# Performance work log

Hardware: AMD Instinct MI355X
Metric: run time of the kernel (lower is better)

## Reference

```python
import jax, jax.numpy as jnp
import numpy as np

D_MODEL = 2048
N_HEADS = 16
D_HEAD = D_MODEL // N_HEADS
B, S = 4, 2048


def setup_inputs() -> dict:
    key = jax.random.key(0)
    ks = jax.random.split(key, 5)
    scale = 1.0 / np.sqrt(D_MODEL)
    return {
        "x": jax.random.normal(ks[0], (B, S, D_MODEL), dtype=jnp.float32),
        "w_qkv": jax.random.normal(ks[1], (D_MODEL, 3 * D_MODEL), dtype=jnp.float32) * scale,
        "b_qkv": jax.random.normal(ks[2], (3 * D_MODEL,), dtype=jnp.float32) * 0.01,
        "w_out": jax.random.normal(ks[3], (D_MODEL, D_MODEL), dtype=jnp.float32) * scale,
        "b_out": jax.random.normal(ks[4], (D_MODEL,), dtype=jnp.float32) * 0.01,
    }


def reference(x, w_qkv, b_qkv, w_out, b_out):
    b, s, d = x.shape
    qkv = x @ w_qkv + b_qkv                      # [b, s, 3d]
    q, k, v = jnp.split(qkv, 3, axis=-1)
    # [b, h, s, dh]
    q = q.reshape(b, s, N_HEADS, D_HEAD).transpose(0, 2, 1, 3)
    k = k.reshape(b, s, N_HEADS, D_HEAD).transpose(0, 2, 1, 3)
    v = v.reshape(b, s, N_HEADS, D_HEAD).transpose(0, 2, 1, 3)
    # past_kv is None -> s_past == s
    scale = 1.0 / np.sqrt(D_HEAD).astype(np.float32)
    scores = jnp.einsum("bhqd,bhkd->bhqk", q, k) * scale  # [b, h, s, s]
    # causal mask: disallow j > i (diagonal = 1 + s_past - s = 1)
    causal = jnp.tril(jnp.ones((s, s), dtype=bool))
    scores = jnp.where(causal, scores, jnp.float32(-jnp.inf))
    attn = jax.nn.softmax(scores, axis=-1)
    out = jnp.einsum("bhqk,bhkd->bhqd", attn, v)          # [b, h, s, dh]
    out = out.transpose(0, 2, 1, 3).reshape(b, s, d)
    out = out @ w_out + b_out
    return out, k, v
```

## Files before the change

### kernel.cpp

```cpp
#include <hip/hip_runtime.h>
#include <hip/hip_bf16.h>
#include <cstdint>

typedef unsigned short u16;
typedef unsigned int u32;
typedef __attribute__((ext_vector_type(4))) float f32x4;
typedef __attribute__((ext_vector_type(8))) __bf16 bf16x8;

#define DEVFN static __device__ __forceinline__

constexpr int Bb = 4, S = 2048, Dm = 2048, H = 16, DH = 128;
constexpr int M  = Bb * S;
constexpr int N3 = 3 * Dm;
constexpr int KK = 2048;
constexpr float ATTN_SCALE = 0.088388347648318447f;
constexpr float LOG2E = 1.4426950408889634f;

DEVFN u16 f2bf(float f) {
  union { float f; u32 u; } v; v.f = f;
  u32 u = v.u;
  return (u16)((u + 0x7fffu + ((u >> 16) & 1u)) >> 16);
}

DEVFN void async16(const void* g, void* l) {
  __builtin_amdgcn_global_load_lds(
      (__attribute__((address_space(1))) unsigned int*)(g),
      (__attribute__((address_space(3))) unsigned int*)(l), 16, 0, 0);
}


DEVFN void transpose_tile(const float* __restrict__ in, u16* __restrict__ out,
                          int R, int C, int bx, int by, int tid) {
  __shared__ float tile[32][33];
  int c0 = bx * 32, r0 = by * 32;
  int tx = tid & 31, ty = tid >> 5;
#pragma unroll
  for (int i = 0; i < 4; i++)
    tile[ty + 8 * i][tx] = in[(size_t)(r0 + ty + 8 * i) * C + c0 + tx];
  __syncthreads();
  int tx2 = (tid & 7) * 4, ty2 = tid >> 3;
  ushort4 o;
  o.x = f2bf(tile[tx2 + 0][ty2]);
  o.y = f2bf(tile[tx2 + 1][ty2]);
  o.z = f2bf(tile[tx2 + 2][ty2]);
  o.w = f2bf(tile[tx2 + 3][ty2]);
  *(ushort4*)(&out[(size_t)(c0 + ty2) * R + r0 + tx2]) = o;
}

__global__ __launch_bounds__(256) void k_prep(
    const float* __restrict__ x, const float* __restrict__ w_qkv,
    const float* __restrict__ w_out, u16* __restrict__ x_bf,
    u16* __restrict__ wqkvT, u16* __restrict__ woutT) {
  const int bid = blockIdx.x, tid = threadIdx.x;
  constexpr int NB_CVT = (M * Dm) / 1024;
  constexpr int NB_T1 = (N3 / 32) * (Dm / 32);
  if (bid < NB_CVT) {
    int i = (bid * 256 + tid) * 4;
    float4 f = *(const float4*)(x + i);
    ushort4 o;
    o.x = f2bf(f.x); o.y = f2bf(f.y); o.z = f2bf(f.z); o.w = f2bf(f.w);
    *(ushort4*)(x_bf + i) = o;
  } else if (bid < NB_CVT + NB_T1) {
    int b2 = bid - NB_CVT;
    transpose_tile(w_qkv, wqkvT, Dm, N3, b2 % (N3 / 32), b2 / (N3 / 32), tid);
  } else {
    int b3 = bid - NB_CVT - NB_T1;
    transpose_tile(w_out, woutT, Dm, Dm, b3 % (Dm / 32), b3 / (Dm / 32), tid);
  }
}


#define RA(buf, half) ((buf) * 65536 + (half) * 16384)
#define RB(buf, half) ((buf) * 65536 + 32768 + (half) * 16384)

#define BARRIER() __builtin_amdgcn_s_barrier()
#define SCHEDB() __builtin_amdgcn_sched_barrier(0)
#define LGK0() { asm volatile("s_waitcnt lgkmcnt(0)" ::: "memory"); __builtin_amdgcn_sched_barrier(0); }
#define VMC0() { asm volatile("s_waitcnt vmcnt(0)" ::: "memory"); __builtin_amdgcn_sched_barrier(0); }

template <int BUF, int QUAD>
DEVFN void ldAq(const char* lds, int wm, int lrow, int lkg, bf16x8 af[4][2]) {
  const char* base = lds + RA(BUF, 0) + wm * 16384;
  const int sw = (lrow & 7) << 4;
#pragma unroll
  for (int mi = 0; mi < 4; mi++) {
    int row = QUAD * 64 + mi * 16 + lrow;
#pragma unroll
    for (int kk = 0; kk < 2; kk++)
      af[mi][kk] = *(const bf16x8*)(base + row * 128 + ((kk * 64 + lkg * 16) ^ sw));
  }
}

template <int BUF, int NS>
DEVFN void ldB(const char* lds, int wn, int lrow, int lkg, bf16x8 b[2][2]) {
  const char* base = lds + RB(BUF, 0) + (wn >> 1) * 16384;
  const int sw = (lrow & 7) << 4;
#pragma unroll
  for (int ni = 0; ni < 2; ni++) {
    int row = (wn & 1) * 64 + NS * 32 + ni * 16 + lrow;
#pragma unroll
    for (int kk = 0; kk < 2; kk++)
      b[ni][kk] = *(const bf16x8*)(base + row * 128 + ((kk * 64 + lkg * 16) ^ sw));
  }
}

template <int MS, int NS>
DEVFN void mmq(f32x4 acc[8][4], bf16x8 af[4][2], bf16x8 b[2][2]) {
  __builtin_amdgcn_s_setprio(1);
#pragma unroll
  for (int kk = 0; kk < 2; kk++)
#pragma unroll
    for (int mi = 0; mi < 4; mi++)
#pragma unroll
      for (int ni = 0; ni < 2; ni++)
        acc[MS * 4 + mi][NS * 2 + ni] = __builtin_amdgcn_mfma_f32_16x16x32_bf16(
            af[mi][kk], b[ni][kk], acc[MS * 4 + mi][NS * 2 + ni], 0, 0, 0);
  __builtin_amdgcn_s_setprio(0);
}

template <int MODE>
__global__ __launch_bounds__(512, 2) void k_gemm(
    const u16* __restrict__ A, const u16* __restrict__ BT,
    const float* __restrict__ bias, float* __restrict__ Cf,
    u16* __restrict__ q_bf, u16* __restrict__ k_bf, u16* __restrict__ v_bfT,
    int N) {
  __shared__ __align__(16) char lds[131072];
  char* ldsc = lds;
  const int tid = threadIdx.x;
  const int wid = tid >> 6, lane = tid & 63;
  const int wm = wid >> 2, wn = wid & 3;
  const int lrow = lane & 15, lkg = lane >> 4;

  const int bid = blockIdx.x;
  const int xcd = bid & 7;
  const int i = bid >> 3;
  const int r = i & 15;
  const int j = i >> 4;
  const int tm0 = (xcd * 4 + (r >> 2)) << 8;
  const int tn0 = (j * 4 + (r & 3)) << 8;

  const int NT = KK >> 6;

  const int srow = tid >> 3;
  const int scol = (((tid & 7) * 16) ^ ((srow & 7) << 4)) >> 1;
  const int dstoff = (tid & ~63) * 16;
  const u16* bA0 = A + (size_t)(tm0 + srow) * KK + scol;
  const u16* bA1 = A + (size_t)(tm0 + 128 + srow) * KK + scol;
  const u16* bB0 = BT + (size_t)(tn0 + srow) * KK + scol;
  const u16* bB1 = BT + (size_t)(tn0 + 128 + srow) * KK + scol;

  auto stage2 = [&](const u16* src, int region) {
    async16(src, ldsc + region + dstoff);
    async16(src + (size_t)64 * KK, ldsc + region + 8192 + dstoff);
  };

  f32x4 acc[8][4] = {};
  bf16x8 afA[4][2], afB[4][2], b0[2][2], b1[2][2];

  stage2(bA0, RA(0, 0));
  stage2(bA1, RA(0, 1));
  stage2(bB0, RB(0, 0));
  stage2(bB1, RB(0, 1));
  VMC0();
  BARRIER();

  for (int it = 0; it < NT / 2; it++) {
    const int t = 2 * it;
    const int t1 = (t + 1) * 64;
    const int t2 = (t + 2 < NT) ? (t + 2) * 64 : 0;

    ldAq<0, 0>(ldsc, wm, lrow, lkg, afA);
    ldB<0, 0>(ldsc, wn, lrow, lkg, b0);
    stage2(bA0 + t1, RA(1, 0));
    stage2(bB0 + t1, RB(1, 0));
    SCHEDB();
    BARRIER(); LGK0();
    mmq<0, 0>(acc, afA, b0);

    ldB<0, 1>(ldsc, wn, lrow, lkg, b1);
    stage2(bA1 + t1, RA(1, 1));
    stage2(bB1 + t1, RB(1, 1));
    SCHEDB();
    BARRIER(); LGK0();
    mmq<0, 1>(acc, afA, b1);

    ldAq<0, 1>(ldsc, wm, lrow, lkg, afB);
    SCHEDB();
    BARRIER(); LGK0();
    mmq<1, 1>(acc, afB, b1);

    VMC0();
    BARRIER();
    mmq<1, 0>(acc, afB, b0);

    ldAq<1, 0>(ldsc, wm, lrow, lkg, afA);
    ldB<1, 0>(ldsc, wn, lrow, lkg, b0);
    stage2(bA0 + t2, RA(0, 0));
    stage2(bB0 + t2, RB(0, 0));
    SCHEDB();
    BARRIER(); LGK0();
    mmq<0, 0>(acc, afA, b0);

    ldB<1, 1>(ldsc, wn, lrow, lkg, b1);
    stage2(bA1 + t2, RA(0, 1));
    stage2(bB1 + t2, RB(0, 1));
    SCHEDB();
    BARRIER(); LGK0();
    mmq<0, 1>(acc, afA, b1);

    ldAq<1, 1>(ldsc, wm, lrow, lkg, afB);
    SCHEDB();
    BARRIER(); LGK0();
    mmq<1, 1>(acc, afB, b1);

    VMC0();
    BARRIER();
    mmq<1, 0>(acc, afB, b0);
  }

  if (MODE == 0) {
#pragma unroll
    for (int mig = 0; mig < 8; mig++) {
      int row = tm0 + wm * 128 + (mig >> 2) * 64 + (mig & 3) * 16 + lkg * 4;
#pragma unroll
      for (int nig = 0; nig < 4; nig++) {
        int col = tn0 + wn * 64 + (nig >> 1) * 32 + (nig & 1) * 16 + lrow;
        float bv = bias[col];
#pragma unroll
        for (int r2 = 0; r2 < 4; r2++)
          Cf[(size_t)(row + r2) * N + col] = acc[mig][nig][r2] + bv;
      }
    }
  } else {
#pragma unroll
    for (int mig = 0; mig < 8; mig++) {
      int row = tm0 + wm * 128 + (mig >> 2) * 64 + (mig & 3) * 16 + lkg * 4;
#pragma unroll
      for (int nig = 0; nig < 4; nig++) {
        int n = tn0 + wn * 64 + (nig >> 1) * 32 + (nig & 1) * 16 + lrow;
        float bv = bias[n];
        int type = n >> 11;
        int d = n & 2047;
        int h = d >> 7, dh = d & 127;
#pragma unroll
        for (int r2 = 0; r2 < 4; r2++) {
          int rr = row + r2;
          int b = rr >> 11, s = rr & 2047;
          float val = acc[mig][nig][r2] + bv;
          size_t idx = ((size_t)(b * H + h) * S + s) * DH + dh;
          if (type == 0) {
            q_bf[idx] = f2bf(val * ATTN_SCALE);
          } else if (type == 1) {
            Cf[(size_t)M * Dm + idx] = val;
            k_bf[idx] = f2bf(val);
          } else {
            Cf[(size_t)2 * M * Dm + idx] = val;
            v_bfT[((size_t)(b * H + h) * DH + dh) * S + s] = f2bf(val);
          }
        }
      }
    }
  }
}

__global__ __launch_bounds__(256, 2) void k_attn(const u16* __restrict__ q_bf,
                                                 const u16* __restrict__ k_bf,
                                                 const u16* __restrict__ v_bfT,
                                                 u16* __restrict__ attn_bf) {
  __shared__ u16 ldsK[2][64 * 128];
  __shared__ u16 ldsV[2][128 * 64];
  __shared__ u16 ldsP[4][32 * 64];

  const int tid = threadIdx.x;
  const int wid = tid >> 6, lane = tid & 63;
  const int lrow = lane & 15, lkg = lane >> 4;

  const int bid = blockIdx.x;
  const int xcd = bid & 7;
  const int ii = bid >> 3;
  const int bh = xcd * 8 + (ii >> 4);
  const int qi = 15 - (ii & 15);
  const int b = bh >> 4, h = bh & 15;
  const int wq0 = qi * 128 + wid * 32;
  const int swz = (lrow & 7) << 4;

  const u16* qp = q_bf + (size_t)bh * S * DH;
  const u16* kp = k_bf + (size_t)bh * S * DH;
  const u16* vp = v_bfT + (size_t)bh * DH * S;

  bf16x8 qf[2][4];
#pragma unroll
  for (int qt = 0; qt < 2; qt++)
#pragma unroll
    for (int kk = 0; kk < 4; kk++)
      qf[qt][kk] = *(const bf16x8*)(qp + (size_t)(wq0 + qt * 16 + lrow) * DH +
                                    kk * 32 + lkg * 8);

  float mr[2][4], lr[2][4];
#pragma unroll
  for (int qt = 0; qt < 2; qt++)
#pragma unroll
    for (int r = 0; r < 4; r++) { mr[qt][r] = -1e30f; lr[qt][r] = 0.f; }
  f32x4 oacc[2][8] = {};

  const int nkb = qi * 2 + 2;

  auto stage = [&](int kb, int buf) {
#pragma unroll
    for (int i = 0; i < 4; i++) {
      int L = i * 4096 + wid * 1024 + lane * 16;
      int krow = L >> 8, kch = (L >> 4) & 15;
      async16(kp + (size_t)(kb * 64 + krow) * DH + ((kch ^ (krow & 7)) * 8),
              (char*)ldsK[buf] + L);
      int vd = L >> 7, vch = (L >> 4) & 7;
      async16(vp + (size_t)vd * S + kb * 64 + ((vch ^ (vd & 7)) * 8),
              (char*)ldsV[buf] + L);
    }
  };

  stage(0, 0);
  asm volatile("s_waitcnt vmcnt(0)" ::: "memory");
  __builtin_amdgcn_s_barrier();

  int cur = 0;
  for (int kb = 0; kb < nkb; kb++) {
    if (kb + 1 < nkb) stage(kb + 1, cur ^ 1);

    if (kb * 64 <= wq0 + 31) {
      const u16* Kc = ldsK[cur];
      const u16* Vc = ldsV[cur];
      f32x4 sacc[2][4] = {};
      __builtin_amdgcn_s_setprio(1);
#pragma unroll
      for (int kt = 0; kt < 4; kt++)
#pragma unroll
        for (int kk = 0; kk < 4; kk++) {
          bf16x8 kf = *(const bf16x8*)((const char*)Kc +
                        (kt * 16 + lrow) * 256 + ((kk * 64 + lkg * 16) ^ swz));
          sacc[0][kt] = __builtin_amdgcn_mfma_f32_16x16x32_bf16(qf[0][kk], kf,
                                                                sacc[0][kt], 0, 0, 0);
          sacc[1][kt] = __builtin_amdgcn_mfma_f32_16x16x32_bf16(qf[1][kk], kf,
                                                                sacc[1][kt], 0, 0, 0);
        }
      __builtin_amdgcn_s_setprio(0);

      if (kb * 64 + 63 > wq0) {
#pragma unroll
        for (int qt = 0; qt < 2; qt++)
#pragma unroll
          for (int kt = 0; kt < 4; kt++) {
            int k = kb * 64 + kt * 16 + lrow;
#pragma unroll
            for (int r = 0; r < 4; r++)
              if (k > wq0 + qt * 16 + lkg * 4 + r) sacc[qt][kt][r] = -1e30f;
          }
      }

      float pm[2][4];
#pragma unroll
      for (int qt = 0; qt < 2; qt++)
#pragma unroll
        for (int r = 0; r < 4; r++)
          pm[qt][r] = fmaxf(fmaxf(sacc[qt][0][r], sacc[qt][1][r]),
                            fmaxf(sacc[qt][2][r], sacc[qt][3][r]));
#pragma unroll
      for (int off = 1; off < 16; off <<= 1)
#pragma unroll
        for (int qt = 0; qt < 2; qt++)
#pragma unroll
          for (int r = 0; r < 4; r++)
            pm[qt][r] = fmaxf(pm[qt][r], __shfl_xor(pm[qt][r], off, 64));

      float dmax = pm[0][0] - mr[0][0];
#pragma unroll
      for (int qt = 0; qt < 2; qt++)
#pragma unroll
        for (int r = 0; r < 4; r++)
          dmax = fmaxf(dmax, pm[qt][r] - mr[qt][r]);
      if (!__all(dmax <= 8.0f)) {
        float sc[2][4];
#pragma unroll
        for (int qt = 0; qt < 2; qt++)
#pragma unroll
          for (int r = 0; r < 4; r++) {
            float mn = fmaxf(mr[qt][r], pm[qt][r]);
            sc[qt][r] = exp2f((mr[qt][r] - mn) * LOG2E);
            mr[qt][r] = mn;
            lr[qt][r] *= sc[qt][r];
          }
#pragma unroll
        for (int qt = 0; qt < 2; qt++)
#pragma unroll
          for (int nd = 0; nd < 8; nd++)
#pragma unroll
            for (int r = 0; r < 4; r++) oacc[qt][nd][r] *= sc[qt][r];
      }

      float rs[2][4] = {};
#pragma unroll
      for (int qt = 0; qt < 2; qt++)
#pragma unroll
        for (int kt = 0; kt < 4; kt++)
#pragma unroll
          for (int r = 0; r < 4; r++) {
            float p = exp2f((sacc[qt][kt][r] - mr[qt][r]) * LOG2E);
            rs[qt][r] += p;
            int prow = qt * 16 + lkg * 4 + r;
            *(u16*)((char*)ldsP[wid] + prow * 128 +
                    (((kt * 16 + lrow) * 2) ^ ((prow & 7) << 4))) = f2bf(p);
          }
#pragma unroll
      for (int off = 1; off < 16; off <<= 1)
#pragma unroll
        for (int qt = 0; qt < 2; qt++)
#pragma unroll
          for (int r = 0; r < 4; r++)
            rs[qt][r] += __shfl_xor(rs[qt][r], off, 64);
#pragma unroll
      for (int qt = 0; qt < 2; qt++)
#pragma unroll
        for (int r = 0; r < 4; r++)
          lr[qt][r] += rs[qt][r];

      asm volatile("s_waitcnt lgkmcnt(0)" ::: "memory");
      bf16x8 pf[2][2];
#pragma unroll
      for (int qt = 0; qt < 2; qt++)
#pragma unroll
        for (int kk = 0; kk < 2; kk++)
          pf[qt][kk] = *(const bf16x8*)((const char*)ldsP[wid] +
                         (qt * 16 + lrow) * 128 + ((kk * 64 + lkg * 16) ^ swz));
      __builtin_amdgcn_s_setprio(1);
#pragma unroll
      for (int nd = 0; nd < 8; nd++) {
        bf16x8 vf0 = *(const bf16x8*)((const char*)Vc +
                       (nd * 16 + lrow) * 128 + ((lkg * 16) ^ swz));
        bf16x8 vf1 = *(const bf16x8*)((const char*)Vc +
                       (nd * 16 + lrow) * 128 + ((64 + lkg * 16) ^ swz));
#pragma unroll
        for (int qt = 0; qt < 2; qt++) {
          oacc[qt][nd] = __builtin_amdgcn_mfma_f32_16x16x32_bf16(pf[qt][0], vf0,
                                                                 oacc[qt][nd], 0, 0, 0);
          oacc[qt][nd] = __builtin_amdgcn_mfma_f32_16x16x32_bf16(pf[qt][1], vf1,
                                                                 oacc[qt][nd], 0, 0, 0);
        }
      }
      __builtin_amdgcn_s_setprio(0);
    }

    asm volatile("s_waitcnt vmcnt(0)" ::: "memory");
    __builtin_amdgcn_s_barrier();
    cur ^= 1;
  }

#pragma unroll
  for (int qt = 0; qt < 2; qt++) {
    float inv[4];
#pragma unroll
    for (int r = 0; r < 4; r++) inv[r] = 1.0f / lr[qt][r];
#pragma unroll
    for (int nd = 0; nd < 8; nd++)
#pragma unroll
      for (int r = 0; r < 4; r++) {
        int q = wq0 + qt * 16 + lkg * 4 + r;
        size_t idx = ((size_t)(b * S + q) * H + h) * DH + nd * 16 + lrow;
        attn_bf[idx] = f2bf(oacc[qt][nd][r] * inv[r]);
      }
  }
}


extern "C" void kernel_launch(void* const* d_in, const int* in_sizes, int n_in,
                              void* d_out, int out_size, void* d_ws, size_t ws_size,
                              hipStream_t stream) {
  const float* x     = (const float*)d_in[0];
  const float* w_qkv = (const float*)d_in[1];
  const float* b_qkv = (const float*)d_in[2];
  const float* w_out = (const float*)d_in[3];
  const float* b_out = (const float*)d_in[4];
  float* out = (float*)d_out;

  char* ws = (char*)d_ws;
  u16* x_bf    = (u16*)ws; ws += (size_t)M * Dm * 2;
  u16* wqkvT   = (u16*)ws; ws += (size_t)N3 * Dm * 2;
  u16* woutT   = (u16*)ws; ws += (size_t)Dm * Dm * 2;
  u16* q_bf    = (u16*)ws; ws += (size_t)M * Dm * 2;
  u16* k_bf    = (u16*)ws; ws += (size_t)M * Dm * 2;
  u16* v_bfT   = (u16*)ws; ws += (size_t)M * Dm * 2;
  u16* attn_bf = (u16*)ws; ws += (size_t)M * Dm * 2;

  constexpr int NB_PREP = (M * Dm) / 1024 + (N3 / 32) * (Dm / 32) +
                          (Dm / 32) * (Dm / 32);
  k_prep<<<NB_PREP, 256, 0, stream>>>(x, w_qkv, w_out, x_bf, wqkvT, woutT);

  k_gemm<1><<<(N3 / 256) * (M / 256), 512, 0, stream>>>(
      x_bf, wqkvT, b_qkv, out, q_bf, k_bf, v_bfT, N3);

  k_attn<<<S / 128 * Bb * H, 256, 0, stream>>>(q_bf, k_bf, v_bfT, attn_bf);

  k_gemm<0><<<(Dm / 256) * (M / 256), 512, 0, stream>>>(
      attn_bf, woutT, b_out, out, nullptr, nullptr, nullptr, Dm);
}
```

Baseline: 545.7 us.

## Split GEMM blocks into sixteen waves with 64x64 per-wave tiles

Both GEMM kernels now launch 1024 threads per block instead of 512. Each of the 16 waves computes a 64x64 output sub-tile instead of 128x64, and each thread stages one 16-byte chunk per LDS region instead of two. LDS fragment loaders and the epilogue indexing are rewritten for the new wave-to-tile mapping. The aim is to lower per-wave register pressure and spread the global-to-LDS copies over more threads, at the cost of more LDS reads per MFMA, less register reuse, and barriers across more waves with only one block per CU.

```diff
diff --git a/kernel.cpp b/kernel.cpp
--- a/kernel.cpp
+++ b/kernel.cpp
@@ -78,48 +78,46 @@
 #define LGK0() { asm volatile("s_waitcnt lgkmcnt(0)" ::: "memory"); __builtin_amdgcn_sched_barrier(0); }
 #define VMC0() { asm volatile("s_waitcnt vmcnt(0)" ::: "memory"); __builtin_amdgcn_sched_barrier(0); }
 
-template <int BUF, int QUAD>
-DEVFN void ldAq(const char* lds, int wm, int lrow, int lkg, bf16x8 af[4][2]) {
-  const char* base = lds + RA(BUF, 0) + wm * 16384;
-  const int sw = (lrow & 7) << 4;
-#pragma unroll
-  for (int mi = 0; mi < 4; mi++) {
-    int row = QUAD * 64 + mi * 16 + lrow;
+template <int BUF, int MH>
+DEVFN void ldAh(const char* lds, int wm, int lrow, int lkg, bf16x8 af[2][2]) {
+  const char* base = lds + RA(BUF, 0);
+#pragma unroll
+  for (int mi = 0; mi < 2; mi++) {
+    int row = wm * 64 + MH * 32 + mi * 16 + lrow;
 #pragma unroll
     for (int kk = 0; kk < 2; kk++)
-      af[mi][kk] = *(const bf16x8*)(base + row * 128 + ((kk * 64 + lkg * 16) ^ sw));
-  }
-}
-
-template <int BUF, int NS>
-DEVFN void ldB(const char* lds, int wn, int lrow, int lkg, bf16x8 b[2][2]) {
-  const char* base = lds + RB(BUF, 0) + (wn >> 1) * 16384;
-  const int sw = (lrow & 7) << 4;
+      af[mi][kk] = *(const bf16x8*)(base + row * 128 + ((kk * 64 + lkg * 16) ^ ((row & 7) << 4)));
+  }
+}
+
+template <int BUF, int NH>
+DEVFN void ldBh(const char* lds, int wn, int lrow, int lkg, bf16x8 b[2][2]) {
+  const char* base = lds + RB(BUF, 0);
 #pragma unroll
   for (int ni = 0; ni < 2; ni++) {
-    int row = (wn & 1) * 64 + NS * 32 + ni * 16 + lrow;
+    int row = wn * 64 + NH * 32 + ni * 16 + lrow;
 #pragma unroll
     for (int kk = 0; kk < 2; kk++)
-      b[ni][kk] = *(const bf16x8*)(base + row * 128 + ((kk * 64 + lkg * 16) ^ sw));
-  }
-}
-
-template <int MS, int NS>
-DEVFN void mmq(f32x4 acc[8][4], bf16x8 af[4][2], bf16x8 b[2][2]) {
+      b[ni][kk] = *(const bf16x8*)(base + row * 128 + ((kk * 64 + lkg * 16) ^ ((row & 7) << 4)));
+  }
+}
+
+template <int MH, int NH>
+DEVFN void mmq(f32x4 acc[4][4], bf16x8 af[2][2], bf16x8 b[2][2]) {
   __builtin_amdgcn_s_setprio(1);
 #pragma unroll
   for (int kk = 0; kk < 2; kk++)
 #pragma unroll
-    for (int mi = 0; mi < 4; mi++)
+    for (int mi = 0; mi < 2; mi++)
 #pragma unroll
       for (int ni = 0; ni < 2; ni++)
-        acc[MS * 4 + mi][NS * 2 + ni] = __builtin_amdgcn_mfma_f32_16x16x32_bf16(
-            af[mi][kk], b[ni][kk], acc[MS * 4 + mi][NS * 2 + ni], 0, 0, 0);
+        acc[MH * 2 + mi][NH * 2 + ni] = __builtin_amdgcn_mfma_f32_16x16x32_bf16(
+            af[mi][kk], b[ni][kk], acc[MH * 2 + mi][NH * 2 + ni], 0, 0, 0);
   __builtin_amdgcn_s_setprio(0);
 }
 
 template <int MODE>
-__global__ __launch_bounds__(512, 2) void k_gemm(
+__global__ __launch_bounds__(1024) void k_gemm(
     const u16* __restrict__ A, const u16* __restrict__ BT,
     const float* __restrict__ bias, float* __restrict__ Cf,
     u16* __restrict__ q_bf, u16* __restrict__ k_bf, u16* __restrict__ v_bfT,
@@ -142,49 +140,47 @@
   const int NT = KK >> 6;
 
   const int srow = tid >> 3;
-  const int scol = (((tid & 7) * 16) ^ ((srow & 7) << 4)) >> 1;
+  const int scol = (((tid & 7) ^ ((tid >> 3) & 7)) << 3);
   const int dstoff = (tid & ~63) * 16;
   const u16* bA0 = A + (size_t)(tm0 + srow) * KK + scol;
   const u16* bA1 = A + (size_t)(tm0 + 128 + srow) * KK + scol;
   const u16* bB0 = BT + (size_t)(tn0 + srow) * KK + scol;
   const u16* bB1 = BT + (size_t)(tn0 + 128 + srow) * KK + scol;
 
-  auto stage2 = [&](const u16* src, int region) {
+  auto stage1 = [&](const u16* src, int region) {
     async16(src, ldsc + region + dstoff);
-    async16(src + (size_t)64 * KK, ldsc + region + 8192 + dstoff);
   };
 
-  f32x4 acc[8][4] = {};
-  bf16x8 afA[4][2], afB[4][2], b0[2][2], b1[2][2];
-
-  stage2(bA0, RA(0, 0));
-  stage2(bA1, RA(0, 1));
-  stage2(bB0, RB(0, 0));
-  stage2(bB1, RB(0, 1));
+  f32x4 acc[4][4] = {};
+  bf16x8 afA[2][2], afB[2][2], b0[2][2], b1[2][2];
+
+  stage1(bA0, RA(0, 0));
+  stage1(bA1, RA(0, 1));
+  stage1(bB0, RB(0, 0));
+  stage1(bB1, RB(0, 1));
   VMC0();
   BARRIER();
 
   for (int it = 0; it < NT / 2; it++) {
-    const int t = 2 * it;
-    const int t1 = (t + 1) * 64;
-    const int t2 = (t + 2 < NT) ? (t + 2) * 64 : 0;
-
-    ldAq<0, 0>(ldsc, wm, lrow, lkg, afA);
-    ldB<0, 0>(ldsc, wn, lrow, lkg, b0);
-    stage2(bA0 + t1, RA(1, 0));
-    stage2(bB0 + t1, RB(1, 0));
+    const int t1 = (2 * it + 1) * 64;
+    const int t2 = (2 * it + 2 < NT) ? (2 * it + 2) * 64 : 0;
+
+    ldAh<0, 0>(ldsc, wm, lrow, lkg, afA);
+    ldBh<0, 0>(ldsc, wn, lrow, lkg, b0);
+    stage1(bA0 + t1, RA(1, 0));
+    stage1(bB0 + t1, RB(1, 0));
     SCHEDB();
     BARRIER(); LGK0();
     mmq<0, 0>(acc, afA, b0);
 
-    ldB<0, 1>(ldsc, wn, lrow, lkg, b1);
-    stage2(bA1 + t1, RA(1, 1));
-    stage2(bB1 + t1, RB(1, 1));
+    ldBh<0, 1>(ldsc, wn, lrow, lkg, b1);
+    stage1(bA1 + t1, RA(1, 1));
+    stage1(bB1 + t1, RB(1, 1));
     SCHEDB();
     BARRIER(); LGK0();
     mmq<0, 1>(acc, afA, b1);
 
-    ldAq<0, 1>(ldsc, wm, lrow, lkg, afB);
+    ldAh<0, 1>(ldsc, wm, lrow, lkg, afB);
     SCHEDB();
     BARRIER(); LGK0();
     mmq<1, 1>(acc, afB, b1);
@@ -193,22 +189,22 @@
     BARRIER();
     mmq<1, 0>(acc, afB, b0);
 
-    ldAq<1, 0>(ldsc, wm, lrow, lkg, afA);
-    ldB<1, 0>(ldsc, wn, lrow, lkg, b0);
-    stage2(bA0 + t2, RA(0, 0));
-    stage2(bB0 + t2, RB(0, 0));
+    ldAh<1, 0>(ldsc, wm, lrow, lkg, afA);
+    ldBh<1, 0>(ldsc, wn, lrow, lkg, b0);
+    stage1(bA0 + t2, RA(0, 0));
+    stage1(bB0 + t2, RB(0, 0));
     SCHEDB();
     BARRIER(); LGK0();
     mmq<0, 0>(acc, afA, b0);
 
-    ldB<1, 1>(ldsc, wn, lrow, lkg, b1);
-    stage2(bA1 + t2, RA(0, 1));
-    stage2(bB1 + t2, RB(0, 1));
+    ldBh<1, 1>(ldsc, wn, lrow, lkg, b1);
+    stage1(bA1 + t2, RA(0, 1));
+    stage1(bB1 + t2, RB(0, 1));
     SCHEDB();
     BARRIER(); LGK0();
     mmq<0, 1>(acc, afA, b1);
 
-    ldAq<1, 1>(ldsc, wm, lrow, lkg, afB);
+    ldAh<1, 1>(ldsc, wm, lrow, lkg, afB);
     SCHEDB();
     BARRIER(); LGK0();
     mmq<1, 1>(acc, afB, b1);
@@ -220,24 +216,24 @@
 
   if (MODE == 0) {
 #pragma unroll
-    for (int mig = 0; mig < 8; mig++) {
-      int row = tm0 + wm * 128 + (mig >> 2) * 64 + (mig & 3) * 16 + lkg * 4;
-#pragma unroll
-      for (int nig = 0; nig < 4; nig++) {
-        int col = tn0 + wn * 64 + (nig >> 1) * 32 + (nig & 1) * 16 + lrow;
+    for (int mi = 0; mi < 4; mi++) {
+      int row = tm0 + wm * 64 + mi * 16 + lkg * 4;
+#pragma unroll
+      for (int ni = 0; ni < 4; ni++) {
+        int col = tn0 + wn * 64 + ni * 16 + lrow;
         float bv = bias[col];
 #pragma unroll
         for (int r2 = 0; r2 < 4; r2++)
-          Cf[(size_t)(row + r2) * N + col] = acc[mig][nig][r2] + bv;
+          Cf[(size_t)(row + r2) * N + col] = acc[mi][ni][r2] + bv;
       }
     }
   } else {
 #pragma unroll
-    for (int mig = 0; mig < 8; mig++) {
-      int row = tm0 + wm * 128 + (mig >> 2) * 64 + (mig & 3) * 16 + lkg * 4;
-#pragma unroll
-      for (int nig = 0; nig < 4; nig++) {
-        int n = tn0 + wn * 64 + (nig >> 1) * 32 + (nig & 1) * 16 + lrow;
+    for (int mi = 0; mi < 4; mi++) {
+      int row = tm0 + wm * 64 + mi * 16 + lkg * 4;
+#pragma unroll
+      for (int ni = 0; ni < 4; ni++) {
+        int n = tn0 + wn * 64 + ni * 16 + lrow;
         float bv = bias[n];
         int type = n >> 11;
         int d = n & 2047;
@@ -246,7 +242,7 @@
         for (int r2 = 0; r2 < 4; r2++) {
           int rr = row + r2;
           int b = rr >> 11, s = rr & 2047;
-          float val = acc[mig][nig][r2] + bv;
+          float val = acc[mi][ni][r2] + bv;
           size_t idx = ((size_t)(b * H + h) * S + s) * DH + dh;
           if (type == 0) {
             q_bf[idx] = f2bf(val * ATTN_SCALE);
@@ -493,11 +489,11 @@
                           (Dm / 32) * (Dm / 32);
   k_prep<<<NB_PREP, 256, 0, stream>>>(x, w_qkv, w_out, x_bf, wqkvT, woutT);
 
-  k_gemm<1><<<(N3 / 256) * (M / 256), 512, 0, stream>>>(
+  k_gemm<1><<<(N3 / 256) * (M / 256), 1024, 0, stream>>>(
       x_bf, wqkvT, b_qkv, out, q_bf, k_bf, v_bfT, N3);
 
   k_attn<<<S / 128 * Bb * H, 256, 0, stream>>>(q_bf, k_bf, v_bfT, attn_bf);
 
-  k_gemm<0><<<(Dm / 256) * (M / 256), 512, 0, stream>>>(
+  k_gemm<0><<<(Dm / 256) * (M / 256), 1024, 0, stream>>>(
       attn_bf, woutT, b_out, out, nullptr, nullptr, nullptr, Dm);
 }
```

Result: slower. 707.6 us (+29.7%).
